# Performance work log

Hardware: AMD Instinct MI355X
Metric: run time of the kernel (lower is better)

Reference implementation:

```python
import jax, jax.numpy as jnp
import numpy as np
from jax import lax

B, N, C = 32, 1024, 768
H_RES, W_RES = 32, 32
NUM_HEADS = 8
CH = C // NUM_HEADS  # 96
SCALE = CH ** -0.5


def setup_inputs() -> dict:
    key = jax.random.key(0)
    k1, k2, k3 = jax.random.split(key, 3)
    x = jax.random.normal(k1, (B, N, C), dtype=jnp.float32)
    # trunc_normal_(std=0.02) approximated by normal * 0.02
    w_qkv = jax.random.normal(k2, (3 * C, C), dtype=jnp.float32) * 0.02
    # conv init: normal(0, sqrt(2/fan_out)), fan_out = 3*3*C/groups = 9
    w_crpe = jax.random.normal(k3, (C, 1, 3, 3), dtype=jnp.float32) * np.sqrt(2.0 / 9.0)
    b_crpe = jnp.zeros((C,), dtype=jnp.float32)
    return {"x": x, "w_qkv": w_qkv, "w_crpe": w_crpe, "b_crpe": b_crpe}


def _forward(x, w_qkv, w_crpe, b_crpe):
    b, n, c = x.shape
    h, ch = NUM_HEADS, CH
    # qkv projection: [B,N,3C] -> [3,B,h,N,Ch]
    qkv = jnp.einsum('bnc,dc->bnd', x, w_qkv)
    qkv = qkv.reshape(b, n, 3, h, ch).transpose(2, 0, 3, 1, 4)
    q, k, v = qkv[0], qkv[1], qkv[2]  # each [B,h,N,Ch]
    # softmax over token dim (dim=2 of [B,h,N,Ch])
    k_softmax = jax.nn.softmax(k, axis=2)
    # dd_trans = k_softmax^T @ v : [B,h,Ch,Ch]
    dd_trans = jnp.einsum('bhnc,bhnd->bhcd', k_softmax, v)
    factor_attn = jnp.einsum('bhnc,bhcd->bhnd', q, dd_trans)  # [B,h,N,Ch]
    # crpe: depthwise 3x3 conv on v reshaped to image layout
    v_img = v.transpose(0, 1, 3, 2).reshape(b, c, H_RES, W_RES)  # B (h Ch) H W
    conv_v = lax.conv_general_dilated(
        v_img, w_crpe, window_strides=(1, 1), padding='SAME',
        feature_group_count=c,
        dimension_numbers=('NCHW', 'OIHW', 'NCHW'))
    conv_v = conv_v + b_crpe[None, :, None, None]
    conv_v = conv_v.reshape(b, h, ch, n).transpose(0, 1, 3, 2)  # [B,h,N,Ch]
    crpe = q * conv_v
    out = SCALE * factor_attn + crpe  # [B,h,N,Ch]
    return out.transpose(0, 2, 1, 3).reshape(b, n, c)


def reference(x, w_qkv, w_crpe, b_crpe):
    return _forward(x, w_qkv, w_crpe, b_crpe)
```

## Files before the change

kernel.cpp:

```cpp
#include <hip/hip_runtime.h>
#include <stdint.h>

#define B_SZ   32
#define N_TOK  1024
#define C_DIM  768
#define HEADS  8
#define CH_DIM 96
#define GM     32768
#define GN     2304
#define GK     768
#define SCALE_F 0.10206207261596577f
#define WHICH_STRIDE 25165824u
#define BH_STRIDE    98304u

typedef __attribute__((ext_vector_type(8))) short short8;
typedef __attribute__((ext_vector_type(8))) unsigned short ushort8;
typedef __attribute__((ext_vector_type(4))) float f32x4;
typedef __attribute__((ext_vector_type(4))) int int4v;

__device__ __forceinline__ float bf2f(unsigned short u) {
  union { unsigned int i; float f; } x; x.i = ((unsigned int)u) << 16; return x.f;
}
__device__ __forceinline__ unsigned short f2bf(float f) {
  union { float f; unsigned int i; } x; x.f = f;
  unsigned int r = x.i + 0x7fffu + ((x.i >> 16) & 1u);
  return (unsigned short)(r >> 16);
}

__device__ __forceinline__ void gload_lds16(const void* g, void* l) {
  __builtin_amdgcn_global_load_lds(
      (const __attribute__((address_space(1))) unsigned int*)g,
      (__attribute__((address_space(3))) unsigned int*)l, 16, 0, 0);
}

__global__ __launch_bounds__(256) void quant_rows(
    const float* __restrict__ x, const float* __restrict__ wq,
    signed char* __restrict__ xq, signed char* __restrict__ wqo,
    float* __restrict__ inv_x, float* __restrict__ inv_w) {
  const int row = blockIdx.x * 4 + (threadIdx.x >> 6);
  const int l = threadIdx.x & 63;
  const float* src; signed char* dst; float* inv; int r;
  if (row < GM) { src = x;  dst = xq;  inv = inv_x; r = row; }
  else { r = row - GM; if (r >= GN) return; src = wq; dst = wqo; inv = inv_w; }

  const float4* s4 = (const float4*)(src + (size_t)r * 768);
  float4 v0 = s4[l], v1 = s4[l + 64], v2 = s4[l + 128];
  float m = fmaxf(fmaxf(fmaxf(fabsf(v0.x), fabsf(v0.y)), fmaxf(fabsf(v0.z), fabsf(v0.w))),
                  fmaxf(fmaxf(fabsf(v1.x), fabsf(v1.y)), fmaxf(fabsf(v1.z), fabsf(v1.w))));
  m = fmaxf(m, fmaxf(fmaxf(fabsf(v2.x), fabsf(v2.y)), fmaxf(fabsf(v2.z), fabsf(v2.w))));
#pragma unroll
  for (int off = 32; off; off >>= 1) m = fmaxf(m, __shfl_xor(m, off));
  const float sc = 127.0f / m;
  if (l == 0) inv[r] = m * (1.0f / 127.0f);

  char4* d4 = (char4*)(dst + (size_t)r * 768);
  char4 o;
  o.x = (signed char)(int)rintf(v0.x * sc); o.y = (signed char)(int)rintf(v0.y * sc);
  o.z = (signed char)(int)rintf(v0.z * sc); o.w = (signed char)(int)rintf(v0.w * sc);
  d4[l] = o;
  o.x = (signed char)(int)rintf(v1.x * sc); o.y = (signed char)(int)rintf(v1.y * sc);
  o.z = (signed char)(int)rintf(v1.z * sc); o.w = (signed char)(int)rintf(v1.w * sc);
  d4[l + 64] = o;
  o.x = (signed char)(int)rintf(v2.x * sc); o.y = (signed char)(int)rintf(v2.y * sc);
  o.z = (signed char)(int)rintf(v2.z * sc); o.w = (signed char)(int)rintf(v2.w * sc);
  d4[l + 128] = o;
}

__global__ __launch_bounds__(512, 4) void qkv_gemm_i8(
    const signed char* __restrict__ xb,
    const signed char* __restrict__ wb,
    const float* __restrict__ inv_x,
    const float* __restrict__ inv_w,
    unsigned short* __restrict__ qkv) {
  __shared__ __align__(16) char lds[2][24576];

  const int t = threadIdx.x, w = t >> 6, l = t & 63;
  const int l15 = l & 15, lhi = l >> 4;

  const int bid = blockIdx.x;
  const int swz = (bid & 7) * 288 + (bid >> 3);
  const int brow = (swz / 9) * 128;
  const int bcol = (swz % 9) * 256;
  const int wr = w >> 2, wc = w & 3;

  const int s_colb = (((l & 3) ^ ((l >> 3) & 3)) << 4);
  const char* gA0 = (const char*)xb + (size_t)brow * 768 + s_colb;
  const char* gB0 = (const char*)wb + (size_t)bcol * 768 + s_colb;

  const int rd_sw = (lhi * 16) ^ (((l15 >> 1) & 3) << 4);
  const int a_off = (wr * 64 + l15) * 64 + rd_sw;
  const int b_off = 8192 + (wc * 64 + l15) * 64 + rd_sw;

  int4v acc[4][4];
#pragma unroll
  for (int m = 0; m < 4; ++m)
#pragma unroll
    for (int n = 0; n < 4; ++n) acc[m][n] = (int4v){0, 0, 0, 0};

  auto STAGE = [&](int bi, int kt) {
    const int rowL = w * 16 + (l >> 2);
    gload_lds16(gA0 + (size_t)rowL * 768 + kt * 64,         &lds[bi][w * 1024]);
    gload_lds16(gB0 + (size_t)rowL * 768 + kt * 64,         &lds[bi][8192 + w * 1024]);
    gload_lds16(gB0 + (size_t)(rowL + 128) * 768 + kt * 64, &lds[bi][8192 + (w + 8) * 1024]);
  };

  auto COMPUTE = [&](int bi) {
    int4v af[4], bf8[4];
#pragma unroll
    for (int n = 0; n < 4; ++n)
      bf8[n] = *(const int4v*)(&lds[bi][b_off + n * 1024]);
#pragma unroll
    for (int m = 0; m < 4; ++m)
      af[m] = *(const int4v*)(&lds[bi][a_off + m * 1024]);
    __builtin_amdgcn_s_setprio(1);
#pragma unroll
    for (int m = 0; m < 4; ++m)
#pragma unroll
      for (int n = 0; n < 4; ++n)
        acc[m][n] = __builtin_amdgcn_mfma_i32_16x16x64_i8(af[m], bf8[n], acc[m][n], 0, 0, 0);
    __builtin_amdgcn_s_setprio(0);
  };

#define SB __builtin_amdgcn_sched_barrier(0)
#define BAR do { SB; __builtin_amdgcn_s_barrier(); SB; } while (0)

  STAGE(0, 0); STAGE(1, 1);
  SB; asm volatile("s_waitcnt vmcnt(3)" ::: "memory");
  BAR;

  for (int kt = 0; kt < 12; ++kt) {
    COMPUTE(kt & 1);
    BAR;
    if (kt < 10) {
      STAGE(kt & 1, kt + 2);
      SB; asm volatile("s_waitcnt vmcnt(3)" ::: "memory");
    } else if (kt == 10) {
      SB; asm volatile("s_waitcnt vmcnt(0)" ::: "memory");
    }
    BAR;
  }

  const int bb = brow / 1024;
#pragma unroll
  for (int m = 0; m < 4; ++m) {
    const int row0 = brow + wr * 64 + m * 16 + lhi * 4;
    const int tok0 = row0 & 1023;
    float ix[4];
#pragma unroll
    for (int r = 0; r < 4; ++r) ix[r] = inv_x[row0 + r];
#pragma unroll
    for (int n = 0; n < 4; ++n) {
      const int col   = bcol + wc * 64 + n * 16 + l15;
      const float dq0 = inv_w[col];
      const int which = col / 768;
      const int hh    = (col % 768) / 96;
      const int ch    = col % 96;
      unsigned short* dst = qkv + (size_t)which * WHICH_STRIDE
                          + ((size_t)(bb * 8 + hh)) * BH_STRIDE + ch;
#pragma unroll
      for (int r = 0; r < 4; ++r) {
        float v = (float)acc[m][n][r] * dq0 * ix[r];
        if (which == 1) v = __expf(v);
        dst[(size_t)(tok0 + r) * 96] = f2bf(v);
      }
    }
  }
#undef BAR
#undef SB
}

__global__ __launch_bounds__(512, 2) void dd_fused(
    const unsigned short* __restrict__ qkv,
    unsigned short* __restrict__ ddT) {
  __shared__ __align__(16) char smem[124416];
  unsigned short* stg = (unsigned short*)smem;
  float* facc = (float*)smem;
  float* fsum = (float*)(smem + 122880);
  float* sinv = (float*)(smem + 123648);

  const int bh = blockIdx.x;
  const int t = threadIdx.x, w = t >> 6, l = t & 63;
  const int l15 = l & 15, lhi = l >> 4;

  unsigned short* myK = stg + w * 7680;
  unsigned short* myV = myK + 3840;
  const int n   = l >> 1;
  const int chh = l & 1;
  const unsigned short* kb = qkv + WHICH_STRIDE     + (size_t)bh * BH_STRIDE;
  const unsigned short* vb = qkv + 2 * WHICH_STRIDE + (size_t)bh * BH_STRIDE;

  f32x4 acc[6][6], accS[6];
#pragma unroll
  for (int mf = 0; mf < 6; ++mf) {
    accS[mf] = (f32x4){0.f, 0.f, 0.f, 0.f};
#pragma unroll
    for (int nf = 0; nf < 6; ++nf) acc[mf][nf] = (f32x4){0.f, 0.f, 0.f, 0.f};
  }
  short8 ones;
#pragma unroll
  for (int j = 0; j < 8; ++j) ones[j] = (short)0x3F80;

  for (int tt = 0; tt < 4; ++tt) {
    const int n0 = w * 128 + tt * 32;
    const size_t g = (size_t)(n0 + n) * 96 + chh * 48;
#pragma unroll
    for (int i = 0; i < 6; ++i) {
      ushort8 k8 = *(const ushort8*)(kb + g + i * 8);
      ushort8 v8 = *(const ushort8*)(vb + g + i * 8);
      const int c0 = chh * 48 + i * 8;
#pragma unroll
      for (int j = 0; j < 8; ++j) {
        myK[(c0 + j) * 40 + n] = k8[j];
        myV[(c0 + j) * 40 + n] = v8[j];
      }
    }
    short8 af[6], bf8[6];
#pragma unroll
    for (int mf = 0; mf < 6; ++mf)
      af[mf] = *(const short8*)((const char*)myK + (mf * 16 + l15) * 80 + lhi * 16);
#pragma unroll
    for (int nf = 0; nf < 6; ++nf)
      bf8[nf] = *(const short8*)((const char*)myV + (nf * 16 + l15) * 80 + lhi * 16);
#pragma unroll
    for (int mf = 0; mf < 6; ++mf) {
#pragma unroll
      for (int nf = 0; nf < 6; ++nf)
        acc[mf][nf] = __builtin_amdgcn_mfma_f32_16x16x32_bf16(af[mf], bf8[nf], acc[mf][nf], 0, 0, 0);
      accS[mf] = __builtin_amdgcn_mfma_f32_16x16x32_bf16(af[mf], ones, accS[mf], 0, 0, 0);
    }
  }

  __syncthreads();
  float* fr  = facc + (w >> 2) * 9600;
  float* fsr = fsum + (w >> 2) * 96;
  for (int ww = 0; ww < 4; ++ww) {
    if ((w & 3) == ww) {
#pragma unroll
      for (int mf = 0; mf < 6; ++mf) {
#pragma unroll
        for (int nf = 0; nf < 6; ++nf) {
          const int c = mf * 16 + lhi * 4, d = nf * 16 + l15;
#pragma unroll
          for (int r = 0; r < 4; ++r) {
            float* p = fr + (size_t)(c + r) * 100 + d;
            if (ww == 0) *p = acc[mf][nf][r]; else *p += acc[mf][nf][r];
          }
        }
        if (l15 == 0) {
          const int c = mf * 16 + lhi * 4;
#pragma unroll
          for (int r = 0; r < 4; ++r) {
            if (ww == 0) fsr[c + r] = accS[mf][r];
            else         fsr[c + r] += accS[mf][r];
          }
        }
      }
    }
    __syncthreads();
  }
  for (int i = t; i < 9600; i += 512) facc[i] += facc[9600 + i];
  if (t < 96) fsum[t] += fsum[96 + t];
  __syncthreads();
  if (t < 96) sinv[t] = 1.0f / fsum[t];
  __syncthreads();

  unsigned short* dst = ddT + (size_t)bh * 9216;
#pragma unroll
  for (int e = 0; e < 18; ++e) {
    const int idx = t * 18 + e;
    const int d = idx / 96, c = idx % 96;
    dst[idx] = f2bf(facc[(size_t)c * 100 + d] * sinv[c]);
  }
}

__global__ __launch_bounds__(256) void factor_conv_p(
    const unsigned short* __restrict__ qkv,
    const unsigned short* __restrict__ ddT,
    const float* __restrict__ wcr,
    const float* __restrict__ bcr,
    float* __restrict__ outb) {
  __shared__ __align__(16) unsigned short sQ[64 * 96];
  __shared__ __align__(16) unsigned short sD[96 * 96];
  __shared__ __align__(16) unsigned short sV[128 * 96];
  __shared__ float sW[96 * 9];
  __shared__ float sBias[96];
  const int half = blockIdx.x, h = blockIdx.y, b = blockIdx.z;
  const int t = threadIdx.x, wv = t >> 6, l = t & 63;
  const int l15 = l & 15, lhi = l >> 4;
  const int bh = b * 8 + h;

  const char* dg = (const char*)ddT + (size_t)bh * 18432;
#pragma unroll
  for (int it = 0; it < 4; ++it)
    gload_lds16(dg + (it * 256 + t) * 16, (char*)sD + it * 4096 + wv * 1024);
  if (wv < 2)
    gload_lds16(dg + (1024 + t) * 16, (char*)sD + 16384 + wv * 1024);
  for (int i = t; i < 960; i += 256) {
    if (i < 864) sW[i] = wcr[(size_t)(h * 96) * 9 + i];
    else         sBias[i - 864] = bcr[h * 96 + (i - 864)];
  }

  const char* qg = (const char*)(qkv + (size_t)bh * BH_STRIDE);
  const char* vg = (const char*)(qkv + 2 * WHICH_STRIDE + (size_t)bh * BH_STRIDE);
  const int wrow = (wv >> 1) * 32;
  const int wcol = (wv & 1) * 48;

  for (int it8 = 0; it8 < 8; ++it8) {
    const int nt = half * 8 + it8;
    const int n0 = nt * 64, y0 = nt * 2;

#pragma unroll
    for (int it = 0; it < 3; ++it)
      gload_lds16(qg + (size_t)n0 * 192 + (it * 256 + t) * 16,
                  (char*)sQ + it * 4096 + wv * 1024);
#pragma unroll
    for (int it = 0; it < 6; ++it) {
      const int f = it * 256 + t;
      const int row = f / 12, ch = f % 12;
      int tok = n0 - 32 + row;
      tok = tok < 0 ? 0 : (tok > 1023 ? 1023 : tok);
      gload_lds16(vg + (size_t)tok * 192 + ch * 16,
                  (char*)sV + it * 4096 + wv * 1024);
    }
    __syncthreads();

    f32x4 acc[2][3];
#pragma unroll
    for (int m = 0; m < 2; ++m)
#pragma unroll
      for (int nn = 0; nn < 3; ++nn) acc[m][nn] = (f32x4){0.f, 0.f, 0.f, 0.f};

#pragma unroll
    for (int ks = 0; ks < 3; ++ks) {
      short8 af[2], bf8[3];
#pragma unroll
      for (int m = 0; m < 2; ++m)
        af[m] = *(const short8*)((const char*)sQ + (wrow + m*16 + l15) * 192 + ks * 64 + lhi * 16);
#pragma unroll
      for (int nn = 0; nn < 3; ++nn)
        bf8[nn] = *(const short8*)((const char*)sD + (wcol + nn*16 + l15) * 192 + ks * 64 + lhi * 16);
#pragma unroll
      for (int m = 0; m < 2; ++m)
#pragma unroll
        for (int nn = 0; nn < 3; ++nn)
          acc[m][nn] = __builtin_amdgcn_mfma_f32_16x16x32_bf16(af[m], bf8[nn], acc[m][nn], 0, 0, 0);
    }

#pragma unroll
    for (int nn = 0; nn < 3; ++nn) {
      const int dc = wcol + nn * 16 + l15;
      float w9[9];
#pragma unroll
      for (int k = 0; k < 9; ++k) w9[k] = sW[dc * 9 + k];
      const float bv = sBias[dc];
#pragma unroll
      for (int m = 0; m < 2; ++m) {
        const int rl0 = wrow + m * 16 + lhi * 4;
        const int x = rl0 & 31, yl = rl0 >> 5;
        float cs[3][6];
#pragma unroll
        for (int dy = 0; dy < 3; ++dy) {
          const int gy = y0 + yl + dy - 1;
          const bool vy = (gy >= 0) && (gy < 32);
#pragma unroll
          for (int i = 0; i < 6; ++i) {
            const int xx = x - 1 + i;
            cs[dy][i] = (vy && xx >= 0 && xx < 32)
                ? bf2f(sV[((yl + dy) * 32 + xx) * 96 + dc]) : 0.f;
          }
        }
#pragma unroll
        for (int r = 0; r < 4; ++r) {
          float conv = bv;
#pragma unroll
          for (int dy = 0; dy < 3; ++dy)
#pragma unroll
            for (int dx = 0; dx < 3; ++dx)
              conv += w9[dy * 3 + dx] * cs[dy][r + dx];
          const int row = rl0 + r;
          const float qv = bf2f(sQ[row * 96 + dc]);
          outb[((size_t)(b * N_TOK + n0 + row)) * C_DIM + h * 96 + dc] =
              SCALE_F * acc[m][nn][r] + qv * conv;
        }
      }
    }
    __syncthreads();
  }
}

extern "C" void kernel_launch(void* const* d_in, const int* in_sizes, int n_in,
                              void* d_out, int out_size, void* d_ws, size_t ws_size,
                              hipStream_t stream) {
  const float* x      = (const float*)d_in[0];
  const float* w_qkv  = (const float*)d_in[1];
  const float* w_crpe = (const float*)d_in[2];
  const float* b_crpe = (const float*)d_in[3];
  float* out = (float*)d_out;

  char* ws = (char*)d_ws;
  signed char*    xq    = (signed char*)ws;
  signed char*    wq    = (signed char*)(ws + 25165824);
  float*          inv_x = (float*)(ws + 27000832);
  float*          inv_w = (float*)(ws + 27131904);
  unsigned short* qkv   = (unsigned short*)(ws + 53870592);
  unsigned short* ddT   = (unsigned short*)(ws + 204865536);

  quant_rows<<<dim3((GM + GN + 3) / 4), 256, 0, stream>>>(
      x, w_qkv, xq, wq, inv_x, inv_w);
  qkv_gemm_i8<<<dim3(2304), 512, 0, stream>>>(xq, wq, inv_x, inv_w, qkv);
  dd_fused<<<dim3(B_SZ * HEADS), 512, 0, stream>>>(qkv, ddT);
  factor_conv_p<<<dim3(2, HEADS, B_SZ), 256, 0, stream>>>(qkv, ddT, w_crpe, b_crpe, out);
}
```

Measured before the change: 216.1 us.

## Reuse V halo rows via ring buffer and raise occupancy hints

The factor/conv kernel used to reload a 4-row V window (with halo) from global memory for every 2-row tile. It now keeps a 6-slot ring buffer of image rows in LDS and stages only the two new rows each iteration, roughly halving V traffic. The launch bounds also gain a min-blocks hint for both kernels, which may force register limits and spills. The ring indexing relies on the slot lifetime working out correctly when rows are overwritten after the trailing barrier.

New measurement: 714.2 us. +230.4%, slower.

```diff
diff --git a/kernel.cpp b/kernel.cpp
--- a/kernel.cpp
+++ b/kernel.cpp
@@ -66,7 +66,7 @@
   d4[l + 128] = o;
 }
 
-__global__ __launch_bounds__(512, 4) void qkv_gemm_i8(
+__global__ __launch_bounds__(512, 6) void qkv_gemm_i8(
     const signed char* __restrict__ xb,
     const signed char* __restrict__ wb,
     const float* __restrict__ inv_x,
@@ -273,7 +273,7 @@
   }
 }
 
-__global__ __launch_bounds__(256) void factor_conv_p(
+__global__ __launch_bounds__(256, 2) void factor_conv_p(
     const unsigned short* __restrict__ qkv,
     const unsigned short* __restrict__ ddT,
     const float* __restrict__ wcr,
@@ -281,7 +281,7 @@
     float* __restrict__ outb) {
   __shared__ __align__(16) unsigned short sQ[64 * 96];
   __shared__ __align__(16) unsigned short sD[96 * 96];
-  __shared__ __align__(16) unsigned short sV[128 * 96];
+  __shared__ __align__(16) unsigned short sV[6 * 32 * 96];
   __shared__ float sW[96 * 9];
   __shared__ float sBias[96];
   const int half = blockIdx.x, h = blockIdx.y, b = blockIdx.z;
@@ -305,23 +305,28 @@
   const int wrow = (wv >> 1) * 32;
   const int wcol = (wv & 1) * 48;
 
+  auto STAGE_ROW = [&](int y) {
+    const int yy = y < 0 ? 0 : (y > 31 ? 31 : y);
+    const int slot = (y + 1) % 6;
+    const char* src = vg + (size_t)yy * 6144;
+    char* dst = (char*)sV + slot * 6144;
+    gload_lds16(src + t * 16, dst + wv * 1024);
+    if (wv < 2)
+      gload_lds16(src + 4096 + t * 16, dst + 4096 + wv * 1024);
+  };
+
+  const int Y0 = half * 16;
+  STAGE_ROW(Y0 - 1); STAGE_ROW(Y0); STAGE_ROW(Y0 + 1); STAGE_ROW(Y0 + 2);
+
   for (int it8 = 0; it8 < 8; ++it8) {
-    const int nt = half * 8 + it8;
-    const int n0 = nt * 64, y0 = nt * 2;
+    const int Y = Y0 + it8 * 2;
+    const int n0 = Y * 32;
 
 #pragma unroll
     for (int it = 0; it < 3; ++it)
       gload_lds16(qg + (size_t)n0 * 192 + (it * 256 + t) * 16,
                   (char*)sQ + it * 4096 + wv * 1024);
-#pragma unroll
-    for (int it = 0; it < 6; ++it) {
-      const int f = it * 256 + t;
-      const int row = f / 12, ch = f % 12;
-      int tok = n0 - 32 + row;
-      tok = tok < 0 ? 0 : (tok > 1023 ? 1023 : tok);
-      gload_lds16(vg + (size_t)tok * 192 + ch * 16,
-                  (char*)sV + it * 4096 + wv * 1024);
-    }
+    if (it8 > 0) { STAGE_ROW(Y + 1); STAGE_ROW(Y + 2); }
     __syncthreads();
 
     f32x4 acc[2][3];
@@ -360,13 +365,14 @@
         float cs[3][6];
 #pragma unroll
         for (int dy = 0; dy < 3; ++dy) {
-          const int gy = y0 + yl + dy - 1;
+          const int gy = Y + yl + dy - 1;
           const bool vy = (gy >= 0) && (gy < 32);
+          const int slot = (gy + 1) % 6;
 #pragma unroll
           for (int i = 0; i < 6; ++i) {
             const int xx = x - 1 + i;
             cs[dy][i] = (vy && xx >= 0 && xx < 32)
-                ? bf2f(sV[((yl + dy) * 32 + xx) * 96 + dc]) : 0.f;
+                ? bf2f(sV[slot * 3072 + xx * 96 + dc]) : 0.f;
           }
         }
 #pragma unroll
```
